# Performance work log

Hardware: AMD Instinct MI355X
Metric: run time of the kernel (lower is better)

The kernel has to match this reference:

```python
import jax, jax.numpy as jnp
from jax import lax
import numpy as np

T, I, H = 8192, 256, 1024  # timesteps, input_dim, hidden_dim


def setup_inputs() -> dict:
    key = jax.random.key(0)
    ks = jax.random.split(key, 7)
    s = 1.0 / np.sqrt(H)  # PyTorch LSTM init scale
    return {
        "sequence": jax.random.normal(ks[0], (T, I), jnp.float32),
        "W_ih": jax.random.uniform(ks[1], (4 * H, I), jnp.float32, -s, s),
        "W_hh": jax.random.uniform(ks[2], (4 * H, H), jnp.float32, -s, s),
        "b_ih": jax.random.uniform(ks[3], (4 * H,), jnp.float32, -s, s),
        "b_hh": jax.random.uniform(ks[4], (4 * H,), jnp.float32, -s, s),
        "W_out": jax.random.uniform(ks[5], (1, H), jnp.float32, -s, s),
        "b_out": jax.random.uniform(ks[6], (1,), jnp.float32, -s, s),
    }


def reference(sequence, W_ih, W_hh, b_ih, b_hh, W_out, b_out):
    hdim = W_hh.shape[1]
    # Precompute input projection for all timesteps in one GEMM: [T, 4H]
    x_gates = sequence @ W_ih.T + (b_ih + b_hh)

    def step(carry, xg):
        h, c = carry
        g = xg + h @ W_hh.T  # [4H], gate order i,f,g,o (PyTorch)
        i, f, gg, o = jnp.split(g, 4)
        i = jax.nn.sigmoid(i)
        f = jax.nn.sigmoid(f)
        gg = jnp.tanh(gg)
        o = jax.nn.sigmoid(o)
        c = f * c + i * gg
        h = o * jnp.tanh(c)
        return (h, c), h

    h0 = jnp.zeros((hdim,), sequence.dtype)
    c0 = jnp.zeros((hdim,), sequence.dtype)
    _, hs = lax.scan(step, (h0, c0), x_gates)  # hs: [T, H]
    out = hs @ W_out.T + b_out  # [T, 1]
    return jax.nn.sigmoid(out)
```

## Files before the change

### kernel.cpp

```cpp
#include <hip/hip_runtime.h>
#include <cstdint>
#include <cstddef>


#define T_STEPS 8192
#define IDIM 256
#define HDIM 1024
#define NWG 64
#define TPB 256
#define ZSTR 164

typedef _Float16 h2_t __attribute__((ext_vector_type(2)));

#if defined(__has_builtin)
#if __has_builtin(__builtin_amdgcn_fdot2)
#define HAS_FDOT2 1
#endif
#endif

__device__ __forceinline__ float fdot2(uint32_t a, uint32_t b, float c) {
#ifdef HAS_FDOT2
  return __builtin_amdgcn_fdot2(__builtin_bit_cast(h2_t, a),
                                __builtin_bit_cast(h2_t, b), c, false);
#else
  const h2_t av = __builtin_bit_cast(h2_t, a);
  const h2_t bv = __builtin_bit_cast(h2_t, b);
  c = fmaf((float)av[0], (float)bv[0], c);
  c = fmaf((float)av[1], (float)bv[1], c);
  return c;
#endif
}
__device__ __forceinline__ uint32_t packf16(float a, float b) {
  h2_t v;
  v[0] = (_Float16)a;
  v[1] = (_Float16)b;
  return __builtin_bit_cast(uint32_t, v);
}
__device__ __forceinline__ float sigmoidf_(float x) {
  return 1.0f / (1.0f + __expf(-x));
}
__device__ __forceinline__ float tanhf_(float x) {
  return 1.0f - 2.0f / (1.0f + __expf(2.0f * x));
}

__global__ __launch_bounds__(TPB, 1) void lstm_persistent(
    const float* __restrict__ seq, const float* __restrict__ Wih,
    const float* __restrict__ Whh, const float* __restrict__ bih,
    const float* __restrict__ bhh, const float* __restrict__ Wout,
    const float* __restrict__ bout, float* __restrict__ out,
    uint32_t* __restrict__ ring) {
  const int wg = blockIdx.x;
  const int tid = threadIdx.x;
  const int w = tid >> 6;
  const int l = tid & 63;
  const int gwid = (wg << 2) | w;

  __shared__ alignas(16) uint32_t zbuf[4][4 * ZSTR];
  __shared__ alignas(16) uint32_t wlds[512];

  {
    float4 wv = *(const float4*)(Wout + tid * 4);
    wlds[tid * 2] = packf16(wv.x, wv.y);
    wlds[tid * 2 + 1] = packf16(wv.z, wv.w);
  }
  const float b_out0 = bout[0];

  const int rl = l >> 2;
  const int q = l & 3;
  const int grow = (rl >> 2) * HDIM + wg * 16 + w * 4 + (rl & 3);
  const float bias_l = bih[grow] + bhh[grow];
  const float* whrow = Whh + (size_t)grow * HDIM;
  const float* wirow = Wih + (size_t)grow * IDIM;
  const int cbase = q * 320;
  uint32_t wreg[160];
#pragma unroll
  for (int j2 = 0; j2 < 160; ++j2) {
    const int c = cbase + 2 * j2;
    float a, b;
    if (c < HDIM) {
      a = whrow[c];
      b = whrow[c + 1];
    } else {
      a = wirow[c - HDIM];
      b = wirow[c - HDIM + 1];
    }
    wreg[j2] = packf16(a, b);
  }

  const int hsoff = 8 * l + 4 * (l / 20);

  __syncthreads();

  uint32_t* const zb = zbuf[w];
  float c_st = 0.0f;
  int dead = 0;

  for (int t = 0; t <= T_STEPS; ++t) {
    if (t < T_STEPS) {
      const float4 xv = *(const float4*)(seq + (size_t)t * IDIM + 4 * l);
      zb[524 + 2 * l] = packf16(xv.x, xv.y);
      zb[525 + 2 * l] = packf16(xv.z, xv.w);
    }

    if (t > 0) {
      const uint64_t want =
          (uint64_t)((t - 1) & 15) * 0x0000000100000001ull;
      const uint64_t msk = 0x0000000F0000000Full;
      const uint64_t* hp =
          (const uint64_t*)(ring + ((t - 1) & 1) * HDIM + 16 * l);
      uint64_t v[8] = {0, 0, 0, 0, 0, 0, 0, 0};
      if (!dead) {
        int guard = 0;
        for (;;) {
#pragma unroll
          for (int k = 0; k < 8; ++k)
            v[k] = __hip_atomic_load(hp + k, __ATOMIC_RELAXED,
                                     __HIP_MEMORY_SCOPE_AGENT);
          bool ok = true;
#pragma unroll
          for (int k = 0; k < 8; ++k) ok = ok && ((v[k] & msk) == want);
          if (ok) break;
          if (++guard > (1 << 20)) { dead = 1; break; }
        }
      }
      uint32_t pk[8];
#pragma unroll
      for (int k = 0; k < 8; ++k)
        pk[k] = packf16(__uint_as_float((uint32_t)v[k]),
                        __uint_as_float((uint32_t)(v[k] >> 32)));
      *(uint4*)(zb + hsoff) = *(const uint4*)(pk);
      *(uint4*)(zb + hsoff + 4) = *(const uint4*)(pk + 4);
    } else {
      const uint4 z4 = {0u, 0u, 0u, 0u};
      *(uint4*)(zb + hsoff) = z4;
      *(uint4*)(zb + hsoff + 4) = z4;
    }
    asm volatile("s_waitcnt lgkmcnt(0)" ::: "memory");
    __builtin_amdgcn_sched_barrier(0);

    if (t < T_STEPS) {
      float ac0 = 0.f, ac1 = 0.f, ac2 = 0.f, ac3 = 0.f;
      const uint32_t* zs = zb + ZSTR * q;
#pragma unroll
      for (int k = 0; k < 40; ++k) {
        const uint4 zv = *(const uint4*)(zs + 4 * k);
        ac0 = fdot2(wreg[4 * k + 0], zv.x, ac0);
        ac1 = fdot2(wreg[4 * k + 1], zv.y, ac1);
        ac2 = fdot2(wreg[4 * k + 2], zv.z, ac2);
        ac3 = fdot2(wreg[4 * k + 3], zv.w, ac3);
      }
      float s = (ac0 + ac1) + (ac2 + ac3);
      s += __shfl_xor(s, 1);
      s += __shfl_xor(s, 2);
      const float g = s + bias_l;
      const int j = l & 3;
      const float gi = __shfl(g, 4 * j);
      const float gf = __shfl(g, 16 + 4 * j);
      const float gg = __shfl(g, 32 + 4 * j);
      const float go = __shfl(g, 48 + 4 * j);
      const float is = sigmoidf_(gi);
      const float fs = sigmoidf_(gf);
      const float gt = tanhf_(gg);
      const float os = sigmoidf_(go);
      c_st = fs * c_st + is * gt;
      const float hv = os * tanhf_(c_st);
      if (l < 4) {
        const uint32_t hb = (__float_as_uint(hv) & ~15u) | (uint32_t)(t & 15);
        __hip_atomic_store(ring + (t & 1) * HDIM + wg * 16 + w * 4 + l, hb,
                           __ATOMIC_RELAXED, __HIP_MEMORY_SCOPE_AGENT);
      }
    }

    if (t > 0 && gwid == ((t - 1) & 255)) {
      const uint4 wv0 = *(const uint4*)(wlds + 8 * l);
      const uint4 wv1 = *(const uint4*)(wlds + 8 * l + 4);
      const uint4 zv0 = *(const uint4*)(zb + hsoff);
      const uint4 zv1 = *(const uint4*)(zb + hsoff + 4);
      float o = 0.f;
      o = fdot2(wv0.x, zv0.x, o);
      o = fdot2(wv0.y, zv0.y, o);
      o = fdot2(wv0.z, zv0.z, o);
      o = fdot2(wv0.w, zv0.w, o);
      o = fdot2(wv1.x, zv1.x, o);
      o = fdot2(wv1.y, zv1.y, o);
      o = fdot2(wv1.z, zv1.z, o);
      o = fdot2(wv1.w, zv1.w, o);
#pragma unroll
      for (int off = 32; off >= 1; off >>= 1) o += __shfl_xor(o, off);
      if (l == 0) out[t - 1] = sigmoidf_(o + b_out0);
    }
  }
}

extern "C" void kernel_launch(void* const* d_in, const int* in_sizes, int n_in,
                              void* d_out, int out_size, void* d_ws, size_t ws_size,
                              hipStream_t stream) {
  const float* seq = (const float*)d_in[0];
  const float* Wih = (const float*)d_in[1];
  const float* Whh = (const float*)d_in[2];
  const float* bih = (const float*)d_in[3];
  const float* bhh = (const float*)d_in[4];
  const float* Wout = (const float*)d_in[5];
  const float* bout = (const float*)d_in[6];

  uint32_t* ring = (uint32_t*)d_ws;

  hipMemsetAsync(d_ws, 0xAA, 2 * HDIM * sizeof(uint32_t), stream);

  lstm_persistent<<<NWG, TPB, 0, stream>>>(seq, Wih, Whh, bih, bhh, Wout, bout,
                                           (float*)d_out, ring);
}
```

Before: 19.42 ms.

## Share the hidden-state staging buffer across the workgroup's waves with a barrier

Each wave previously polled and packed the entire 1024-element hidden vector into its own LDS copy. Now the four waves split the polling, each thread loading two 64-bit words, and write into one shared double-buffered LDS tile, synchronized by __syncthreads. This cuts redundant global atomic-load traffic per step by four, but adds a workgroup barrier on the critical serial path.

```diff
diff --git a/kernel.cpp b/kernel.cpp
--- a/kernel.cpp
+++ b/kernel.cpp
@@ -55,7 +55,7 @@
   const int l = tid & 63;
   const int gwid = (wg << 2) | w;
 
-  __shared__ alignas(16) uint32_t zbuf[4][4 * ZSTR];
+  __shared__ alignas(16) uint32_t zbuf[2][4 * ZSTR];
   __shared__ alignas(16) uint32_t wlds[512];
 
   {
@@ -87,56 +87,49 @@
     wreg[j2] = packf16(a, b);
   }
 
-  const int hsoff = 8 * l + 4 * (l / 20);
+  const int hstage = 2 * tid + 4 * (tid / 80);
+  const int hout = 8 * l + 4 * (l / 20);
 
   __syncthreads();
 
-  uint32_t* const zb = zbuf[w];
   float c_st = 0.0f;
   int dead = 0;
 
   for (int t = 0; t <= T_STEPS; ++t) {
-    if (t < T_STEPS) {
-      const float4 xv = *(const float4*)(seq + (size_t)t * IDIM + 4 * l);
-      zb[524 + 2 * l] = packf16(xv.x, xv.y);
-      zb[525 + 2 * l] = packf16(xv.z, xv.w);
+    uint32_t* const zb = zbuf[t & 1];
+
+    if (t < T_STEPS && tid < 64) {
+      const float4 xv = *(const float4*)(seq + (size_t)t * IDIM + 4 * tid);
+      zb[524 + 2 * tid] = packf16(xv.x, xv.y);
+      zb[525 + 2 * tid] = packf16(xv.z, xv.w);
     }
 
     if (t > 0) {
-      const uint64_t want =
-          (uint64_t)((t - 1) & 15) * 0x0000000100000001ull;
+      const uint64_t want = (uint64_t)((t - 1) & 15) * 0x0000000100000001ull;
       const uint64_t msk = 0x0000000F0000000Full;
       const uint64_t* hp =
-          (const uint64_t*)(ring + ((t - 1) & 1) * HDIM + 16 * l);
-      uint64_t v[8] = {0, 0, 0, 0, 0, 0, 0, 0};
+          (const uint64_t*)(ring + ((t - 1) & 1) * HDIM + 4 * tid);
+      uint64_t v0 = 0, v1 = 0;
       if (!dead) {
         int guard = 0;
         for (;;) {
-#pragma unroll
-          for (int k = 0; k < 8; ++k)
-            v[k] = __hip_atomic_load(hp + k, __ATOMIC_RELAXED,
-                                     __HIP_MEMORY_SCOPE_AGENT);
-          bool ok = true;
-#pragma unroll
-          for (int k = 0; k < 8; ++k) ok = ok && ((v[k] & msk) == want);
-          if (ok) break;
+          v0 = __hip_atomic_load(hp + 0, __ATOMIC_RELAXED,
+                                 __HIP_MEMORY_SCOPE_AGENT);
+          v1 = __hip_atomic_load(hp + 1, __ATOMIC_RELAXED,
+                                 __HIP_MEMORY_SCOPE_AGENT);
+          if (((v0 & msk) == want) && ((v1 & msk) == want)) break;
           if (++guard > (1 << 20)) { dead = 1; break; }
         }
       }
-      uint32_t pk[8];
-#pragma unroll
-      for (int k = 0; k < 8; ++k)
-        pk[k] = packf16(__uint_as_float((uint32_t)v[k]),
-                        __uint_as_float((uint32_t)(v[k] >> 32)));
-      *(uint4*)(zb + hsoff) = *(const uint4*)(pk);
-      *(uint4*)(zb + hsoff + 4) = *(const uint4*)(pk + 4);
+      zb[hstage] = packf16(__uint_as_float((uint32_t)v0),
+                           __uint_as_float((uint32_t)(v0 >> 32)));
+      zb[hstage + 1] = packf16(__uint_as_float((uint32_t)v1),
+                               __uint_as_float((uint32_t)(v1 >> 32)));
     } else {
-      const uint4 z4 = {0u, 0u, 0u, 0u};
-      *(uint4*)(zb + hsoff) = z4;
-      *(uint4*)(zb + hsoff + 4) = z4;
-    }
-    asm volatile("s_waitcnt lgkmcnt(0)" ::: "memory");
-    __builtin_amdgcn_sched_barrier(0);
+      zb[hstage] = 0u;
+      zb[hstage + 1] = 0u;
+    }
+    __syncthreads();
 
     if (t < T_STEPS) {
       float ac0 = 0.f, ac1 = 0.f, ac2 = 0.f, ac3 = 0.f;
@@ -174,8 +167,8 @@
     if (t > 0 && gwid == ((t - 1) & 255)) {
       const uint4 wv0 = *(const uint4*)(wlds + 8 * l);
       const uint4 wv1 = *(const uint4*)(wlds + 8 * l + 4);
-      const uint4 zv0 = *(const uint4*)(zb + hsoff);
-      const uint4 zv1 = *(const uint4*)(zb + hsoff + 4);
+      const uint4 zv0 = *(const uint4*)(zb + hout);
+      const uint4 zv1 = *(const uint4*)(zb + hout + 4);
       float o = 0.f;
       o = fdot2(wv0.x, zv0.x, o);
       o = fdot2(wv0.y, zv0.y, o);
```

Measured after the change: 21.01 ms. 8.2% more time.
